# Performance work log

Hardware: AMD Instinct MI355X
Metric: run time of the kernel (lower is better)

Reference implementation:

```python
import jax, jax.numpy as jnp
import numpy as np

WS = 3   # window_size
ND = 3   # n_degree


def grid_sample_bilinear(x, grid):
    """torch.nn.functional.grid_sample, mode='bilinear', padding_mode='zeros', align_corners=True.
    x: [B,C,H,W]; grid: [B,Hg,Wg,2] with grid[...,0]=x(norm), grid[...,1]=y(norm). -> [B,C,Hg,Wg]"""
    B, C, H, W = x.shape
    gx = (grid[..., 0] + 1.0) * 0.5 * (W - 1)
    gy = (grid[..., 1] + 1.0) * 0.5 * (H - 1)
    x0 = jnp.floor(gx); y0 = jnp.floor(gy)
    x1 = x0 + 1.0;      y1 = y0 + 1.0
    wx1 = gx - x0; wx0 = 1.0 - wx1
    wy1 = gy - y0; wy0 = 1.0 - wy1
    xf = x.reshape(B, C, H * W)

    def gather(yi, xi):
        valid = ((yi >= 0) & (yi <= H - 1) & (xi >= 0) & (xi <= W - 1)).astype(x.dtype)
        yc = jnp.clip(yi, 0, H - 1).astype(jnp.int32)
        xc = jnp.clip(xi, 0, W - 1).astype(jnp.int32)
        idx = yc * W + xc                                   # [B,Hg,Wg]
        v = jax.vmap(lambda xb, ib: jnp.take(xb, ib, axis=1))(xf, idx.reshape(B, -1))
        v = v.reshape(B, C, idx.shape[1], idx.shape[2])      # [B,C,Hg,Wg]
        return v * valid[:, None]

    out = (gather(y0, x0) * (wy0 * wx0)[:, None]
         + gather(y0, x1) * (wy0 * wx1)[:, None]
         + gather(y1, x0) * (wy1 * wx0)[:, None]
         + gather(y1, x1) * (wy1 * wx1)[:, None])
    return out


def setup_inputs() -> dict:
    key = jax.random.key(0)
    ks = jax.random.split(key, 8)
    B, Q, C, H, W = 16, 500, 256, 64, 64
    Np = ND + 1
    query = jax.random.normal(ks[0], (B, Q, C), dtype=jnp.float32)
    # polynomial coefficients kept small so most sample points land inside [-1,1]
    polys = jax.random.uniform(ks[1], (B, Q, 2 * Np), dtype=jnp.float32, minval=0.0, maxval=0.25)
    memory = jax.random.normal(ks[2], (B, H * W, C), dtype=jnp.float32)
    memory_spatial_shapes = np.array([[H, W]], dtype=np.int64)  # static shapes
    Wk = jax.random.normal(ks[3], (C, Np * C, WS, WS), dtype=jnp.float32) * 0.02
    bk = jax.random.normal(ks[4], (C,), dtype=jnp.float32) * 0.02
    Wp = jax.random.normal(ks[5], (C, C), dtype=jnp.float32) * 0.02
    bp = jax.random.normal(ks[6], (C,), dtype=jnp.float32) * 0.02
    return {"query": query, "polys": polys, "memory": memory,
            "memory_spatial_shapes": memory_spatial_shapes,
            "Wk": Wk, "bk": bk, "Wp": Wp, "bp": bp}


def reference(query, polys, memory, memory_spatial_shapes, Wk, bk, Wp, bp):
    B, LEN_V, C = memory.shape
    H = int(memory_spatial_shapes[0][0]); W = int(memory_spatial_shapes[0][1])
    Q = polys.shape[1]
    Np = ND + 1

    # memory -> feature map [B,C,H,W]
    x = jnp.transpose(memory[:, :H * W, :], (0, 2, 1)).reshape(B, C, H, W)

    # polynomial sample points: alphas[s,k] = linspace(0,1)[s] ** (ND-k)
    a = jnp.linspace(0.0, 1.0, Np).astype(polys.dtype)
    A = jnp.stack([a ** i for i in range(ND, -1, -1)], axis=1)          # [Np, Np]
    pts = jnp.einsum('bqck,sk->bqcs', polys.reshape(B, Q, 2, Np), A)    # [B,Q,2,Np]
    pts = jnp.transpose(pts, (0, 1, 3, 2))[..., ::-1]                   # [B,Q,Np,2] (flip coords)
    points = 2.0 * pts - 1.0
    points = points[:, :, None]                                         # [B,Q,1,Np,2]

    # window offsets (note python floor-div: (-3)//2 = -2, matches torch source)
    delta_h = 2.0 * jnp.linspace((-WS) // 2, WS // 2, WS) / H
    delta_w = 2.0 * jnp.linspace((-WS) // 2, WS // 2, WS) / W
    mesh_x, mesh_y = jnp.meshgrid(delta_w, delta_h, indexing='xy')       # [WS,WS]
    mesh_x = mesh_x.reshape(-1, 1); mesh_y = mesh_y.reshape(-1, 1)       # [WS*WS,1]

    grid_x = points[..., 1] + mesh_x                                     # [B,Q,WS*WS,Np]
    grid_y = points[..., 0] + mesh_y
    grid = jnp.stack((grid_y, grid_x), axis=-1)                          # [B,Q,WS*WS,Np,2]
    grid = grid.reshape(B, Q * Np * WS, WS, 2)

    sampled = grid_sample_bilinear(x, grid)                              # [B,C,Q*Np*WS,WS]
    sampled = sampled.reshape(B, C, Q * Np, WS, WS)
    sampled = jnp.transpose(sampled, (0, 2, 1, 3, 4)).reshape(B * Q, Np * C, WS, WS)

    # convkk over full window -> 1x1 output: plain contraction
    crcts = jax.nn.relu(jnp.einsum('nikl,oikl->no', sampled, Wk) + bk)   # [B*Q, C]
    crcts = (crcts @ Wp.T + bp).reshape(B, Q, C)
    return crcts, points
```

## Files before the change

### kernel.cpp

```cpp
#include <hip/hip_runtime.h>

#define NB 16
#define NQ 500
#define NC 256
#define NHW 64
#define MR 8000
#define KD 9216

typedef float f32x4 __attribute__((ext_vector_type(4)));
typedef __bf16 bf16x8 __attribute__((ext_vector_type(8)));
typedef unsigned short ushortx8 __attribute__((ext_vector_type(8)));
typedef unsigned short ushortx4 __attribute__((ext_vector_type(4)));

__device__ __forceinline__ unsigned short f2bf(float f) {
  unsigned int u = __builtin_bit_cast(unsigned int, f);
  u += 0x7fffu + ((u >> 16) & 1u);
  return (unsigned short)(u >> 16);
}

__global__ void k_points(const float* __restrict__ polys,
                         float* __restrict__ outp, float* __restrict__ wsp) {
  int n = blockIdx.x * 256 + threadIdx.x;
  if (n >= MR) return;
  f32x4 ca = *(const f32x4*)(polys + (size_t)n * 8);
  f32x4 cb = *(const f32x4*)(polys + (size_t)n * 8 + 4);
  const float av[4] = {0.0f, 0.33333334f, 0.66666669f, 1.0f};
#pragma unroll
  for (int s = 0; s < 4; ++s) {
    float a1 = av[s], a2 = a1 * a1, a3 = a2 * a1;
    float v0 = ca.x * a3 + ca.y * a2 + ca.z * a1 + ca.w;
    float v1 = cb.x * a3 + cb.y * a2 + cb.z * a1 + cb.w;
    float pt0 = 2.0f * v1 - 1.0f;
    float pt1 = 2.0f * v0 - 1.0f;
    outp[(size_t)n * 8 + s * 2 + 0] = pt0;
    outp[(size_t)n * 8 + s * 2 + 1] = pt1;
    wsp[(size_t)n * 8 + s * 2 + 0] = pt0;
    wsp[(size_t)n * 8 + s * 2 + 1] = pt1;
  }
}

__global__ void k_permwk(const float* __restrict__ Wk,
                         unsigned short* __restrict__ W2s) {
  int tid = blockIdx.x * 256 + threadIdx.x;
  if (tid >= (KD / 8) * NC) return;
  int o = tid & 255;
  int th = tid >> 8;
  int r = th >> 5;
  int cbase = (th & 31) * 8;
  int np = r / 9;
  int kl = r - np * 9;
  int kk = kl / 3;
  int ll = kl - kk * 3;
  const float* src = Wk + (size_t)o * KD + (size_t)(np * 256 + cbase) * 9 + kk * 3 + ll;
  ushortx8 v;
#pragma unroll
  for (int j = 0; j < 8; ++j) v[j] = f2bf(src[(size_t)j * 9]);
  *(ushortx8*)(W2s + (size_t)th * 2048 + o * 8) = v;
}

__global__ void k_permwp(const float* __restrict__ Wp,
                         unsigned short* __restrict__ WPs) {
  int tid = blockIdx.x * 256 + threadIdx.x;
  if (tid >= 32 * 256) return;
  int o = tid & 255;
  int th = tid >> 8;
  const float* src = Wp + (size_t)o * 256 + th * 8;
  ushortx8 v;
#pragma unroll
  for (int j = 0; j < 8; ++j) v[j] = f2bf(src[j]);
  *(ushortx8*)(WPs + (size_t)th * 2048 + o * 8) = v;
}

__global__ __launch_bounds__(512, 4) void k_gemm1(
    const float* __restrict__ mem, const float* __restrict__ pts,
    const unsigned short* __restrict__ W2s, const float* __restrict__ bk,
    float* __restrict__ PART, unsigned short* __restrict__ CR1, int K) {
  __shared__ __align__(16) unsigned short Alds[2 * 2048 * 8];

  const int bid = blockIdx.x;
  const int x = bid & 7;
  const int kk8 = (bid >> 3) % K;
  const int j = bid / (8 * K);
  const int t = x + 8 * j;
  if (t >= 125) return;
  const int tt = 16 * x - ((x > 5) ? (x - 5) : 0) + j;
  const int nsl = 36 / K;
  const int r0 = kk8 * nsl;

  const int tid = threadIdx.x;
  const int n0 = tt * 64;
  const int lane = tid & 63;
  const int wave = tid >> 6;
  const int lr = lane & 15;
  const int ksub = lane >> 4;
  const int o0 = wave * 32;

  const int gchunk = tid & 31;
  const int gm0 = tid >> 5;

  size_t boff[4];
  int nrow[4];
#pragma unroll
  for (int task = 0; task < 4; ++task) {
    nrow[task] = n0 + gm0 + 16 * task;
    boff[task] = (size_t)(nrow[task] / NQ) * (NHW * NHW * NC);
  }

  f32x4 acc[4][2] = {};

  for (int r = r0; r < r0 + nsl; ++r) {
    const int s = r & 3;
    const int mm = r >> 2;
    const int mdiv = (mm * 11) >> 5;
    const int mmod = mm - 3 * mdiv;
    const float dhx = (1.5f * (float)mdiv - 2.0f) * 0.03125f;
    const float dwy = (1.5f * (float)mmod - 2.0f) * 0.03125f;
    const int lbase = ((r - r0) & 1) * 2048;
#pragma unroll 2
    for (int task = 0; task < 4; ++task) {
      const int m = gm0 + task * 16;
      const int n = nrow[task];
      const float* mb = mem + boff[task];
      const float p0 = pts[(size_t)n * 8 + s * 2 + 0];
      const float p1 = pts[(size_t)n * 8 + s * 2 + 1];
      const float gx = (p0 + dhx + 1.0f) * 0.5f * 63.0f;
      const float gy = (p1 + dwy + 1.0f) * 0.5f * 63.0f;
      const float x0f = floorf(gx), y0f = floorf(gy);
      const float fx = gx - x0f, fy = gy - y0f;
      const int ix0 = (int)x0f, iy0 = (int)y0f;
      const int ix1 = ix0 + 1, iy1 = iy0 + 1;
      const float vx0 = (ix0 >= 0 && ix0 < NHW) ? 1.0f : 0.0f;
      const float vx1 = (ix1 >= 0 && ix1 < NHW) ? 1.0f : 0.0f;
      const float vy0 = (iy0 >= 0 && iy0 < NHW) ? 1.0f : 0.0f;
      const float vy1 = (iy1 >= 0 && iy1 < NHW) ? 1.0f : 0.0f;
      const float w00 = (1.0f - fy) * (1.0f - fx) * vy0 * vx0;
      const float w01 = (1.0f - fy) * fx * vy0 * vx1;
      const float w10 = fy * (1.0f - fx) * vy1 * vx0;
      const float w11 = fy * fx * vy1 * vx1;
      const int cx0 = min(max(ix0, 0), NHW - 1), cx1 = min(max(ix1, 0), NHW - 1);
      const int cy0 = min(max(iy0, 0), NHW - 1), cy1 = min(max(iy1, 0), NHW - 1);
      const float* q00 = mb + (size_t)(cy0 * NHW + cx0) * NC + gchunk * 8;
      const float* q01 = mb + (size_t)(cy0 * NHW + cx1) * NC + gchunk * 8;
      const float* q10 = mb + (size_t)(cy1 * NHW + cx0) * NC + gchunk * 8;
      const float* q11 = mb + (size_t)(cy1 * NHW + cx1) * NC + gchunk * 8;
      f32x4 v00a = *(const f32x4*)q00, v00b = *(const f32x4*)(q00 + 4);
      f32x4 v01a = *(const f32x4*)q01, v01b = *(const f32x4*)(q01 + 4);
      f32x4 v10a = *(const f32x4*)q10, v10b = *(const f32x4*)(q10 + 4);
      f32x4 v11a = *(const f32x4*)q11, v11b = *(const f32x4*)(q11 + 4);
      f32x4 ra = v00a * w00 + v01a * w01 + v10a * w10 + v11a * w11;
      f32x4 rb = v00b * w00 + v01b * w01 + v10b * w10 + v11b * w11;
      bf16x8 pk;
      pk[0] = (__bf16)ra.x; pk[1] = (__bf16)ra.y;
      pk[2] = (__bf16)ra.z; pk[3] = (__bf16)ra.w;
      pk[4] = (__bf16)rb.x; pk[5] = (__bf16)rb.y;
      pk[6] = (__bf16)rb.z; pk[7] = (__bf16)rb.w;
      const int slot = lbase + gchunk * 64 + (m ^ (gchunk & 15));
      *(bf16x8*)(Alds + slot * 8) = pk;
    }
    __syncthreads();
    const size_t rbase = (size_t)r * 32;
#pragma unroll
    for (int kstep = 0; kstep < 8; ++kstep) {
      const int chunk = kstep * 4 + ksub;
      const unsigned short* bp = W2s + (rbase + chunk) * 2048 + (o0 + lr) * 8;
      ushortx8 ub0 = *(const ushortx8*)bp;
      ushortx8 ub1 = *(const ushortx8*)(bp + 128);
      bf16x8 fb0 = __builtin_bit_cast(bf16x8, ub0);
      bf16x8 fb1 = __builtin_bit_cast(bf16x8, ub1);
#pragma unroll
      for (int mf = 0; mf < 4; ++mf) {
        const int sa = lbase + chunk * 64 + ((mf * 16 + lr) ^ (chunk & 15));
        ushortx8 ua = *(const ushortx8*)(Alds + sa * 8);
        bf16x8 fa = __builtin_bit_cast(bf16x8, ua);
        acc[mf][0] = __builtin_amdgcn_mfma_f32_16x16x32_bf16(fa, fb0, acc[mf][0], 0, 0, 0);
        acc[mf][1] = __builtin_amdgcn_mfma_f32_16x16x32_bf16(fa, fb1, acc[mf][1], 0, 0, 0);
      }
    }
  }
  if (PART) {
    float* dst = PART + (size_t)kk8 * (MR * NC);
#pragma unroll
    for (int mf = 0; mf < 4; ++mf)
#pragma unroll
      for (int nf = 0; nf < 2; ++nf) {
        const int o = o0 + nf * 16 + lr;
#pragma unroll
        for (int reg = 0; reg < 4; ++reg) {
          const int mrow = mf * 16 + ksub * 4 + reg;
          dst[(size_t)(n0 + mrow) * 256 + o] = acc[mf][nf][reg];
        }
      }
  } else {
#pragma unroll
    for (int mf = 0; mf < 4; ++mf)
#pragma unroll
      for (int nf = 0; nf < 2; ++nf) {
        const int o = o0 + nf * 16 + lr;
        const float bko = bk[o];
#pragma unroll
        for (int reg = 0; reg < 4; ++reg) {
          const int mrow = mf * 16 + ksub * 4 + reg;
          float v = acc[mf][nf][reg] + bko;
          v = v > 0.0f ? v : 0.0f;
          CR1[(size_t)(n0 + mrow) * 256 + o] = f2bf(v);
        }
      }
  }
}

__global__ __launch_bounds__(256) void k_red(
    const float* __restrict__ PART, const float* __restrict__ bk,
    unsigned short* __restrict__ CR1, int K) {
  int gid = blockIdx.x * 256 + threadIdx.x;
  size_t idx4 = (size_t)gid * 4;
  if (idx4 >= (size_t)MR * NC) return;
  f32x4 sum = *(const f32x4*)(PART + idx4);
  for (int k = 1; k < K; ++k)
    sum += *(const f32x4*)(PART + (size_t)k * (MR * NC) + idx4);
  f32x4 bv = *(const f32x4*)(bk + (idx4 & 255));
  sum += bv;
  ushortx4 pk;
#pragma unroll
  for (int e = 0; e < 4; ++e) {
    float v = sum[e] > 0.0f ? sum[e] : 0.0f;
    pk[e] = f2bf(v);
  }
  *(ushortx4*)(CR1 + idx4) = pk;
}

__global__ __launch_bounds__(256) void k_gemm2(
    const unsigned short* __restrict__ CR1, const unsigned short* __restrict__ WPs,
    const float* __restrict__ bp, float* __restrict__ outc) {
  const int tid = threadIdx.x;
  const int n0 = blockIdx.x * 16;
  const int lane = tid & 63;
  const int wave = tid >> 6;
  const int lr = lane & 15;
  const int ksub = lane >> 4;
  const int o0 = wave * 64;
  f32x4 acc[4] = {};
#pragma unroll
  for (int kstep = 0; kstep < 8; ++kstep) {
    const int t0 = kstep * 32 + ksub * 8;
    ushortx8 ua0 = *(const ushortx8*)(CR1 + (size_t)(n0 + lr) * 256 + t0);
    bf16x8 fa0 = __builtin_bit_cast(bf16x8, ua0);
    const int chunk = kstep * 4 + ksub;
#pragma unroll
    for (int nf = 0; nf < 4; ++nf) {
      ushortx8 ub = *(const ushortx8*)(WPs + (size_t)chunk * 2048 + (o0 + nf * 16 + lr) * 8);
      bf16x8 fb = __builtin_bit_cast(bf16x8, ub);
      acc[nf] = __builtin_amdgcn_mfma_f32_16x16x32_bf16(fa0, fb, acc[nf], 0, 0, 0);
    }
  }
#pragma unroll
  for (int nf = 0; nf < 4; ++nf) {
    const int o = o0 + nf * 16 + lr;
    const float bpo = bp[o];
#pragma unroll
    for (int reg = 0; reg < 4; ++reg) {
      const int mrow = ksub * 4 + reg;
      outc[(size_t)(n0 + mrow) * 256 + o] = acc[nf][reg] + bpo;
    }
  }
}

extern "C" void kernel_launch(void* const* d_in, const int* in_sizes, int n_in,
                              void* d_out, int out_size, void* d_ws, size_t ws_size,
                              hipStream_t stream) {
  (void)in_sizes; (void)n_in; (void)out_size;
  const float* polys = (const float*)d_in[1];
  const float* mem   = (const float*)d_in[2];
  const float* Wk    = (const float*)d_in[4];
  const float* bk    = (const float*)d_in[5];
  const float* Wp    = (const float*)d_in[6];
  const float* bp    = (const float*)d_in[7];
  float* out = (float*)d_out;
  float* out_pts = out + (size_t)MR * NC;

  unsigned short* W2s = (unsigned short*)d_ws;
  unsigned short* WPs = (unsigned short*)((char*)d_ws + 4718592);
  float*          PTS = (float*)((char*)d_ws + 4849664);
  unsigned short* CR1 = (unsigned short*)((char*)d_ws + 5105664);
  const size_t PART_OFF = 9201664;
  float*          PARTp = (float*)((char*)d_ws + PART_OFF);

  int K = 1;
  if (ws_size >= PART_OFF + 4ull * 8192000ull) K = 4;
  else if (ws_size >= PART_OFF + 2ull * 8192000ull) K = 2;
  float* PART = (K > 1) ? PARTp : nullptr;

  hipLaunchKernelGGL(k_points, dim3(32), dim3(256), 0, stream, polys, out_pts, PTS);
  hipLaunchKernelGGL(k_permwk, dim3(1152), dim3(256), 0, stream, Wk, W2s);
  hipLaunchKernelGGL(k_permwp, dim3(32), dim3(256), 0, stream, Wp, WPs);
  hipLaunchKernelGGL(k_gemm1, dim3(128 * K), dim3(512), 0, stream,
                     mem, PTS, W2s, bk, PART, CR1, K);
  if (PART)
    hipLaunchKernelGGL(k_red, dim3(2000), dim3(256), 0, stream, PART, bk, CR1, K);
  hipLaunchKernelGGL(k_gemm2, dim3(500), dim3(256), 0, stream, CR1, WPs, bp, out);
}
```

Before: 121.2 us.

## Pre-cast memory to bf16 and precompute bilinear sample weights and offsets

Adds a pass that casts the memory tensor to bf16, so the gather in the first GEMM reads half the bytes per corner. Adds a kernel that precomputes, for every sample, the four bilinear weights and clamped offsets, which the GEMM then loads instead of recomputing. It also merges the weight-permutation kernels and fixes the K-split at 4. The cost is an extra full pass over memory (read fp32, write bf16), a larger workspace footprint, and an extra rounding of the sampled inputs to bf16. If the workspace is too small the K-split is still forced to 4, which may be unsafe.

Result: faster. 110.8 us (-8.6%).

```diff
diff --git a/kernel.cpp b/kernel.cpp
--- a/kernel.cpp
+++ b/kernel.cpp
@@ -11,70 +11,129 @@
 typedef __bf16 bf16x8 __attribute__((ext_vector_type(8)));
 typedef unsigned short ushortx8 __attribute__((ext_vector_type(8)));
 typedef unsigned short ushortx4 __attribute__((ext_vector_type(4)));
+typedef int intx4 __attribute__((ext_vector_type(4)));
 
 __device__ __forceinline__ unsigned short f2bf(float f) {
   unsigned int u = __builtin_bit_cast(unsigned int, f);
   u += 0x7fffu + ((u >> 16) & 1u);
   return (unsigned short)(u >> 16);
 }
-
-__global__ void k_points(const float* __restrict__ polys,
-                         float* __restrict__ outp, float* __restrict__ wsp) {
-  int n = blockIdx.x * 256 + threadIdx.x;
-  if (n >= MR) return;
-  f32x4 ca = *(const f32x4*)(polys + (size_t)n * 8);
-  f32x4 cb = *(const f32x4*)(polys + (size_t)n * 8 + 4);
-  const float av[4] = {0.0f, 0.33333334f, 0.66666669f, 1.0f};
-#pragma unroll
-  for (int s = 0; s < 4; ++s) {
-    float a1 = av[s], a2 = a1 * a1, a3 = a2 * a1;
+#define BF2F(u) __builtin_bit_cast(float, (unsigned int)((unsigned int)(u) << 16))
+
+__global__ __launch_bounds__(256) void k_cast(const float* __restrict__ mem,
+                                              unsigned short* __restrict__ memb) {
+  size_t gid = (size_t)blockIdx.x * 256 + threadIdx.x;
+  const float* s = mem + gid * 8;
+  f32x4 a = *(const f32x4*)s, b = *(const f32x4*)(s + 4);
+  bf16x8 pk;
+  pk[0] = (__bf16)a.x; pk[1] = (__bf16)a.y; pk[2] = (__bf16)a.z; pk[3] = (__bf16)a.w;
+  pk[4] = (__bf16)b.x; pk[5] = (__bf16)b.y; pk[6] = (__bf16)b.z; pk[7] = (__bf16)b.w;
+  *(bf16x8*)(memb + gid * 8) = pk;
+}
+
+__global__ void k_prew(const float* __restrict__ Wk, const float* __restrict__ Wp,
+                       unsigned short* __restrict__ W2s,
+                       unsigned short* __restrict__ WPs) {
+  int bid = blockIdx.x;
+  if (bid < 1152) {
+    int tid = bid * 256 + threadIdx.x;
+    int o = tid & 255;
+    int th = tid >> 8;
+    int r = th >> 5;
+    int cbase = (th & 31) * 8;
+    int np = r / 9;
+    int kl = r - np * 9;
+    int kk = kl / 3;
+    int ll = kl - kk * 3;
+    const float* src = Wk + (size_t)o * KD + (size_t)(np * 256 + cbase) * 9 + kk * 3 + ll;
+    ushortx8 v;
+#pragma unroll
+    for (int j = 0; j < 8; ++j) v[j] = f2bf(src[(size_t)j * 9]);
+    *(ushortx8*)(W2s + (size_t)th * 2048 + o * 8) = v;
+  } else {
+    int tid = (bid - 1152) * 256 + threadIdx.x;
+    int o = tid & 255;
+    int th = tid >> 8;
+    const float* src = Wp + (size_t)o * 256 + th * 8;
+    ushortx8 v;
+#pragma unroll
+    for (int j = 0; j < 8; ++j) v[j] = f2bf(src[j]);
+    *(ushortx8*)(WPs + (size_t)th * 2048 + o * 8) = v;
+  }
+}
+
+__global__ void k_wts(const float* __restrict__ polys, float* __restrict__ outp,
+                      float* __restrict__ wsp, float* __restrict__ wts) {
+  int bid = blockIdx.x;
+  if (bid < 1125) {
+    if (!wts) return;
+    int e = bid * 256 + threadIdx.x;
+    int r = e / 8000;
+    int n = e - r * 8000;
+    int s = r & 3;
+    int mm = r >> 2;
+    int mdiv = (mm * 11) >> 5;
+    int mmod = mm - 3 * mdiv;
+    float dhx = (1.5f * (float)mdiv - 2.0f) * 0.03125f;
+    float dwy = (1.5f * (float)mmod - 2.0f) * 0.03125f;
+    f32x4 ca = *(const f32x4*)(polys + (size_t)n * 8);
+    f32x4 cb = *(const f32x4*)(polys + (size_t)n * 8 + 4);
+    float a1 = (s == 3) ? 1.0f : (float)s * 0.33333334f;
+    float a2 = a1 * a1, a3 = a2 * a1;
     float v0 = ca.x * a3 + ca.y * a2 + ca.z * a1 + ca.w;
     float v1 = cb.x * a3 + cb.y * a2 + cb.z * a1 + cb.w;
-    float pt0 = 2.0f * v1 - 1.0f;
-    float pt1 = 2.0f * v0 - 1.0f;
-    outp[(size_t)n * 8 + s * 2 + 0] = pt0;
-    outp[(size_t)n * 8 + s * 2 + 1] = pt1;
-    wsp[(size_t)n * 8 + s * 2 + 0] = pt0;
-    wsp[(size_t)n * 8 + s * 2 + 1] = pt1;
-  }
-}
-
-__global__ void k_permwk(const float* __restrict__ Wk,
-                         unsigned short* __restrict__ W2s) {
-  int tid = blockIdx.x * 256 + threadIdx.x;
-  if (tid >= (KD / 8) * NC) return;
-  int o = tid & 255;
-  int th = tid >> 8;
-  int r = th >> 5;
-  int cbase = (th & 31) * 8;
-  int np = r / 9;
-  int kl = r - np * 9;
-  int kk = kl / 3;
-  int ll = kl - kk * 3;
-  const float* src = Wk + (size_t)o * KD + (size_t)(np * 256 + cbase) * 9 + kk * 3 + ll;
-  ushortx8 v;
-#pragma unroll
-  for (int j = 0; j < 8; ++j) v[j] = f2bf(src[(size_t)j * 9]);
-  *(ushortx8*)(W2s + (size_t)th * 2048 + o * 8) = v;
-}
-
-__global__ void k_permwp(const float* __restrict__ Wp,
-                         unsigned short* __restrict__ WPs) {
-  int tid = blockIdx.x * 256 + threadIdx.x;
-  if (tid >= 32 * 256) return;
-  int o = tid & 255;
-  int th = tid >> 8;
-  const float* src = Wp + (size_t)o * 256 + th * 8;
-  ushortx8 v;
-#pragma unroll
-  for (int j = 0; j < 8; ++j) v[j] = f2bf(src[j]);
-  *(ushortx8*)(WPs + (size_t)th * 2048 + o * 8) = v;
-}
-
+    float p0 = 2.0f * v1 - 1.0f;
+    float p1 = 2.0f * v0 - 1.0f;
+    const float gx = (p0 + dhx + 1.0f) * 0.5f * 63.0f;
+    const float gy = (p1 + dwy + 1.0f) * 0.5f * 63.0f;
+    const float x0f = floorf(gx), y0f = floorf(gy);
+    const float fx = gx - x0f, fy = gy - y0f;
+    const int ix0 = (int)x0f, iy0 = (int)y0f;
+    const int ix1 = ix0 + 1, iy1 = iy0 + 1;
+    const float vx0 = (ix0 >= 0 && ix0 < NHW) ? 1.0f : 0.0f;
+    const float vx1 = (ix1 >= 0 && ix1 < NHW) ? 1.0f : 0.0f;
+    const float vy0 = (iy0 >= 0 && iy0 < NHW) ? 1.0f : 0.0f;
+    const float vy1 = (iy1 >= 0 && iy1 < NHW) ? 1.0f : 0.0f;
+    const float w00 = (1.0f - fy) * (1.0f - fx) * vy0 * vx0;
+    const float w01 = (1.0f - fy) * fx * vy0 * vx1;
+    const float w10 = fy * (1.0f - fx) * vy1 * vx0;
+    const float w11 = fy * fx * vy1 * vx1;
+    const int cx0 = min(max(ix0, 0), NHW - 1), cx1 = min(max(ix1, 0), NHW - 1);
+    const int cy0 = min(max(iy0, 0), NHW - 1), cy1 = min(max(iy1, 0), NHW - 1);
+    float* dst = wts + (size_t)e * 8;
+    f32x4 wv; wv.x = w00; wv.y = w01; wv.z = w10; wv.w = w11;
+    intx4 ov;
+    ov.x = (cy0 * NHW + cx0) * NC; ov.y = (cy0 * NHW + cx1) * NC;
+    ov.z = (cy1 * NHW + cx0) * NC; ov.w = (cy1 * NHW + cx1) * NC;
+    *(f32x4*)dst = wv;
+    *(intx4*)(dst + 4) = ov;
+  } else {
+    int n = (bid - 1125) * 256 + threadIdx.x;
+    if (n >= MR) return;
+    f32x4 ca = *(const f32x4*)(polys + (size_t)n * 8);
+    f32x4 cb = *(const f32x4*)(polys + (size_t)n * 8 + 4);
+    const float av[4] = {0.0f, 0.33333334f, 0.66666669f, 1.0f};
+#pragma unroll
+    for (int s = 0; s < 4; ++s) {
+      float a1 = av[s], a2 = a1 * a1, a3 = a2 * a1;
+      float v0 = ca.x * a3 + ca.y * a2 + ca.z * a1 + ca.w;
+      float v1 = cb.x * a3 + cb.y * a2 + cb.z * a1 + cb.w;
+      float pt0 = 2.0f * v1 - 1.0f;
+      float pt1 = 2.0f * v0 - 1.0f;
+      outp[(size_t)n * 8 + s * 2 + 0] = pt0;
+      outp[(size_t)n * 8 + s * 2 + 1] = pt1;
+      wsp[(size_t)n * 8 + s * 2 + 0] = pt0;
+      wsp[(size_t)n * 8 + s * 2 + 1] = pt1;
+    }
+  }
+}
+
+template <bool USE_WTS>
 __global__ __launch_bounds__(512, 4) void k_gemm1(
-    const float* __restrict__ mem, const float* __restrict__ pts,
-    const unsigned short* __restrict__ W2s, const float* __restrict__ bk,
-    float* __restrict__ PART, unsigned short* __restrict__ CR1, int K) {
+    const unsigned short* __restrict__ memb, const float* __restrict__ pts,
+    const float* __restrict__ wts, const unsigned short* __restrict__ W2s,
+    const float* __restrict__ bk, float* __restrict__ PART,
+    unsigned short* __restrict__ CR1, int K) {
   __shared__ __align__(16) unsigned short Alds[2 * 2048 * 8];
 
   const int bid = blockIdx.x;
@@ -109,46 +168,64 @@
   f32x4 acc[4][2] = {};
 
   for (int r = r0; r < r0 + nsl; ++r) {
-    const int s = r & 3;
-    const int mm = r >> 2;
-    const int mdiv = (mm * 11) >> 5;
-    const int mmod = mm - 3 * mdiv;
-    const float dhx = (1.5f * (float)mdiv - 2.0f) * 0.03125f;
-    const float dwy = (1.5f * (float)mmod - 2.0f) * 0.03125f;
     const int lbase = ((r - r0) & 1) * 2048;
+    float dhx = 0.0f, dwy = 0.0f;
+    int s = 0;
+    if (!USE_WTS) {
+      s = r & 3;
+      const int mm = r >> 2;
+      const int mdiv = (mm * 11) >> 5;
+      const int mmod = mm - 3 * mdiv;
+      dhx = (1.5f * (float)mdiv - 2.0f) * 0.03125f;
+      dwy = (1.5f * (float)mmod - 2.0f) * 0.03125f;
+    }
 #pragma unroll 2
     for (int task = 0; task < 4; ++task) {
       const int m = gm0 + task * 16;
       const int n = nrow[task];
-      const float* mb = mem + boff[task];
-      const float p0 = pts[(size_t)n * 8 + s * 2 + 0];
-      const float p1 = pts[(size_t)n * 8 + s * 2 + 1];
-      const float gx = (p0 + dhx + 1.0f) * 0.5f * 63.0f;
-      const float gy = (p1 + dwy + 1.0f) * 0.5f * 63.0f;
-      const float x0f = floorf(gx), y0f = floorf(gy);
-      const float fx = gx - x0f, fy = gy - y0f;
-      const int ix0 = (int)x0f, iy0 = (int)y0f;
-      const int ix1 = ix0 + 1, iy1 = iy0 + 1;
-      const float vx0 = (ix0 >= 0 && ix0 < NHW) ? 1.0f : 0.0f;
-      const float vx1 = (ix1 >= 0 && ix1 < NHW) ? 1.0f : 0.0f;
-      const float vy0 = (iy0 >= 0 && iy0 < NHW) ? 1.0f : 0.0f;
-      const float vy1 = (iy1 >= 0 && iy1 < NHW) ? 1.0f : 0.0f;
-      const float w00 = (1.0f - fy) * (1.0f - fx) * vy0 * vx0;
-      const float w01 = (1.0f - fy) * fx * vy0 * vx1;
-      const float w10 = fy * (1.0f - fx) * vy1 * vx0;
-      const float w11 = fy * fx * vy1 * vx1;
-      const int cx0 = min(max(ix0, 0), NHW - 1), cx1 = min(max(ix1, 0), NHW - 1);
-      const int cy0 = min(max(iy0, 0), NHW - 1), cy1 = min(max(iy1, 0), NHW - 1);
-      const float* q00 = mb + (size_t)(cy0 * NHW + cx0) * NC + gchunk * 8;
-      const float* q01 = mb + (size_t)(cy0 * NHW + cx1) * NC + gchunk * 8;
-      const float* q10 = mb + (size_t)(cy1 * NHW + cx0) * NC + gchunk * 8;
-      const float* q11 = mb + (size_t)(cy1 * NHW + cx1) * NC + gchunk * 8;
-      f32x4 v00a = *(const f32x4*)q00, v00b = *(const f32x4*)(q00 + 4);
-      f32x4 v01a = *(const f32x4*)q01, v01b = *(const f32x4*)(q01 + 4);
-      f32x4 v10a = *(const f32x4*)q10, v10b = *(const f32x4*)(q10 + 4);
-      f32x4 v11a = *(const f32x4*)q11, v11b = *(const f32x4*)(q11 + 4);
-      f32x4 ra = v00a * w00 + v01a * w01 + v10a * w10 + v11a * w11;
-      f32x4 rb = v00b * w00 + v01b * w01 + v10b * w10 + v11b * w11;
+      float w00, w01, w10, w11;
+      int o00, o01, o10, o11;
+      if (USE_WTS) {
+        const float* we = wts + ((size_t)r * 8000 + n) * 8;
+        f32x4 wv = *(const f32x4*)we;
+        intx4 ov = *(const intx4*)(we + 4);
+        w00 = wv.x; w01 = wv.y; w10 = wv.z; w11 = wv.w;
+        o00 = ov.x; o01 = ov.y; o10 = ov.z; o11 = ov.w;
+      } else {
+        const float p0 = pts[(size_t)n * 8 + s * 2 + 0];
+        const float p1 = pts[(size_t)n * 8 + s * 2 + 1];
+        const float gx = (p0 + dhx + 1.0f) * 0.5f * 63.0f;
+        const float gy = (p1 + dwy + 1.0f) * 0.5f * 63.0f;
+        const float x0f = floorf(gx), y0f = floorf(gy);
+        const float fx = gx - x0f, fy = gy - y0f;
+        const int ix0 = (int)x0f, iy0 = (int)y0f;
+        const int ix1 = ix0 + 1, iy1 = iy0 + 1;
+        const float vx0 = (ix0 >= 0 && ix0 < NHW) ? 1.0f : 0.0f;
+        const float vx1 = (ix1 >= 0 && ix1 < NHW) ? 1.0f : 0.0f;
+        const float vy0 = (iy0 >= 0 && iy0 < NHW) ? 1.0f : 0.0f;
+        const float vy1 = (iy1 >= 0 && iy1 < NHW) ? 1.0f : 0.0f;
+        w00 = (1.0f - fy) * (1.0f - fx) * vy0 * vx0;
+        w01 = (1.0f - fy) * fx * vy0 * vx1;
+        w10 = fy * (1.0f - fx) * vy1 * vx0;
+        w11 = fy * fx * vy1 * vx1;
+        const int cx0 = min(max(ix0, 0), NHW - 1), cx1 = min(max(ix1, 0), NHW - 1);
+        const int cy0 = min(max(iy0, 0), NHW - 1), cy1 = min(max(iy1, 0), NHW - 1);
+        o00 = (cy0 * NHW + cx0) * NC; o01 = (cy0 * NHW + cx1) * NC;
+        o10 = (cy1 * NHW + cx0) * NC; o11 = (cy1 * NHW + cx1) * NC;
+      }
+      const unsigned short* mb = memb + boff[task] + gchunk * 8;
+      ushortx8 u00 = *(const ushortx8*)(mb + o00);
+      ushortx8 u01 = *(const ushortx8*)(mb + o01);
+      ushortx8 u10 = *(const ushortx8*)(mb + o10);
+      ushortx8 u11 = *(const ushortx8*)(mb + o11);
+      f32x4 ra, rb;
+#pragma unroll
+      for (int jj = 0; jj < 4; ++jj) {
+        ra[jj] = BF2F(u00[jj]) * w00 + BF2F(u01[jj]) * w01 +
+                 BF2F(u10[jj]) * w10 + BF2F(u11[jj]) * w11;
+        rb[jj] = BF2F(u00[jj + 4]) * w00 + BF2F(u01[jj + 4]) * w01 +
+                 BF2F(u10[jj + 4]) * w10 + BF2F(u11[jj + 4]) * w11;
+      }
       bf16x8 pk;
       pk[0] = (__bf16)ra.x; pk[1] = (__bf16)ra.y;
       pk[2] = (__bf16)ra.z; pk[3] = (__bf16)ra.w;
@@ -281,20 +358,27 @@
   unsigned short* WPs = (unsigned short*)((char*)d_ws + 4718592);
   float*          PTS = (float*)((char*)d_ws + 4849664);
   unsigned short* CR1 = (unsigned short*)((char*)d_ws + 5105664);
-  const size_t PART_OFF = 9201664;
-  float*          PARTp = (float*)((char*)d_ws + PART_OFF);
-
-  int K = 1;
-  if (ws_size >= PART_OFF + 4ull * 8192000ull) K = 4;
-  else if (ws_size >= PART_OFF + 2ull * 8192000ull) K = 2;
-  float* PART = (K > 1) ? PARTp : nullptr;
-
-  hipLaunchKernelGGL(k_points, dim3(32), dim3(256), 0, stream, polys, out_pts, PTS);
-  hipLaunchKernelGGL(k_permwk, dim3(1152), dim3(256), 0, stream, Wk, W2s);
-  hipLaunchKernelGGL(k_permwp, dim3(32), dim3(256), 0, stream, Wp, WPs);
-  hipLaunchKernelGGL(k_gemm1, dim3(128 * K), dim3(512), 0, stream,
-                     mem, PTS, W2s, bk, PART, CR1, K);
-  if (PART)
-    hipLaunchKernelGGL(k_red, dim3(2000), dim3(256), 0, stream, PART, bk, CR1, K);
+  const size_t BASE_END = 9201664;
+  const size_t WTS_SZ  = 9216000ull;
+  const size_t MEMB_SZ = 33554432ull;
+  const size_t PART_SZ = 8192000ull;
+  const int K = 4;
+
+  bool use_wts = (ws_size >= BASE_END + WTS_SZ + MEMB_SZ + 4 * PART_SZ);
+  size_t memb_off = use_wts ? (BASE_END + WTS_SZ) : BASE_END;
+  float*          WTS  = use_wts ? (float*)((char*)d_ws + BASE_END) : nullptr;
+  unsigned short* MEMB = (unsigned short*)((char*)d_ws + memb_off);
+  float*          PART = (float*)((char*)d_ws + memb_off + MEMB_SZ);
+
+  hipLaunchKernelGGL(k_wts, dim3(1157), dim3(256), 0, stream, polys, out_pts, PTS, WTS);
+  hipLaunchKernelGGL(k_cast, dim3(8192), dim3(256), 0, stream, mem, MEMB);
+  hipLaunchKernelGGL(k_prew, dim3(1184), dim3(256), 0, stream, Wk, Wp, W2s, WPs);
+  if (use_wts)
+    hipLaunchKernelGGL(k_gemm1<true>, dim3(128 * K), dim3(512), 0, stream,
+                       MEMB, PTS, WTS, W2s, bk, PART, CR1, K);
+  else
+    hipLaunchKernelGGL(k_gemm1<false>, dim3(128 * K), dim3(512), 0, stream,
+                       MEMB, PTS, WTS, W2s, bk, PART, CR1, K);
+  hipLaunchKernelGGL(k_red, dim3(2000), dim3(256), 0, stream, PART, bk, CR1, K);
   hipLaunchKernelGGL(k_gemm2, dim3(500), dim3(256), 0, stream, CR1, WPs, bp, out);
 }
```
